# Performance work log

Measured on AMD Instinct MI355X. Metric: run time of the kernel, lower is better.

Reference implementation:

```python
import jax, jax.numpy as jnp
import numpy as np
from jax import lax

B, C, H, W = 8, 128, 128, 128
KW = 9                      # conv window width (w == h == 9)
PW = (KW - 1) // 2


def _make_kernel(key):
    # torch kaiming_normal_(fan_out) on weight (C,1,KW,C): fan_out = C * KW * C
    std = float(np.sqrt(2.0 / (C * KW * C)))
    # stored directly in WIO layout: [KW, C_in, C_out]
    return (jax.random.normal(key, (KW, C, C), dtype=jnp.float32) * std)


def setup_inputs() -> dict:
    key = jax.random.key(0)
    kx, k1, k2, k3, k4 = jax.random.split(key, 5)
    x = jax.random.normal(kx, (B, C, H, W), dtype=jnp.float32)
    return {
        "x": x,
        "k_td": _make_kernel(k1),
        "k_dt": _make_kernel(k2),
        "k_lr": _make_kernel(k3),
        "k_rl": _make_kernel(k4),
    }


def _row_conv(y, K):
    # y: [B, W, C] -> 1D conv along W, full channel mixing, no bias
    return lax.conv_general_dilated(
        y, K, window_strides=(1,), padding=[(PW, PW)],
        dimension_numbers=("NWC", "WIO", "NWC"))


def _dir_scan(x, K, reverse):
    # x: [B, H, W, C]; sequential recurrence along axis 1:
    #   row[i] = row[i] + relu(conv(row[i-1]))   (row[i-1] already updated)
    if reverse:
        x = x[:, ::-1]
    def step(prev, cur):
        new = cur + jax.nn.relu(_row_conv(prev, K))
        return new, new
    first = x[:, 0]
    _, rest = lax.scan(step, first, jnp.moveaxis(x[:, 1:], 1, 0))
    out = jnp.concatenate([first[:, None], jnp.moveaxis(rest, 0, 1)], axis=1)
    if reverse:
        out = out[:, ::-1]
    return out


def reference(x, k_td, k_dt, k_lr, k_rl):
    y = jnp.transpose(x, (0, 2, 3, 1))        # [B, H, W, C]
    y = _dir_scan(y, k_td, reverse=False)      # top -> down
    y = _dir_scan(y, k_dt, reverse=True)       # down -> top
    yt = jnp.swapaxes(y, 1, 2)                 # [B, W, H, C]
    yt = _dir_scan(yt, k_lr, reverse=False)    # left -> right
    yt = _dir_scan(yt, k_rl, reverse=True)     # right -> left
    y = jnp.swapaxes(yt, 1, 2)
    return jnp.transpose(y, (0, 3, 1, 2))      # back to [B, C, H, W]
```

## Files before the change

### kernel.cpp

```cpp
#include <hip/hip_runtime.h>

#define B_   8
#define C_   128
#define HW_  128
#define KW_  9
#define BLKS 8
#define POSB 16
#define ROWS 24
#define STRD 136
#define BUFE (ROWS * STRD)
#define THREADS 512

typedef __bf16 bf16x8 __attribute__((ext_vector_type(8)));
typedef float  floatx4 __attribute__((ext_vector_type(4)));
typedef unsigned long long u64;

__device__ __forceinline__ unsigned short bf16rn(float f) {
  union { float f; unsigned u; } x; x.f = f;
  return (unsigned short)((x.u + 0x7fffu + ((x.u >> 16) & 1u)) >> 16);
}

__global__ __launch_bounds__(256) void nchw_to_nhwc(const float* __restrict__ x,
                                                    float* __restrict__ y) {
  __shared__ float tile[32][33];
  const int blk = blockIdx.x;
  const int b = blk >> 7, h = blk & 127;
  const int tx = threadIdx.x & 31, ty = threadIdx.x >> 5;
  for (int t = 0; t < 16; ++t) {
    const int c0 = (t >> 2) * 32, w0 = (t & 3) * 32;
#pragma unroll
    for (int i = 0; i < 4; ++i) {
      const int c = c0 + ty + i * 8;
      tile[ty + i * 8][tx] = x[(((long)b * C_ + c) * HW_ + h) * HW_ + w0 + tx];
    }
    __syncthreads();
#pragma unroll
    for (int i = 0; i < 4; ++i) {
      const int w = w0 + ty + i * 8;
      y[(((long)b * HW_ + h) * HW_ + w) * C_ + c0 + tx] = tile[tx][ty + i * 8];
    }
    __syncthreads();
  }
}

__global__ __launch_bounds__(256) void nhwc_to_nchw(const float* __restrict__ y,
                                                    float* __restrict__ out) {
  __shared__ float tile[32][33];
  const int blk = blockIdx.x;
  const int b = blk >> 7, h = blk & 127;
  const int tx = threadIdx.x & 31, ty = threadIdx.x >> 5;
  for (int t = 0; t < 16; ++t) {
    const int w0 = (t >> 2) * 32, c0 = (t & 3) * 32;
#pragma unroll
    for (int i = 0; i < 4; ++i) {
      const int w = w0 + ty + i * 8;
      tile[ty + i * 8][tx] = y[(((long)b * HW_ + h) * HW_ + w) * C_ + c0 + tx];
    }
    __syncthreads();
#pragma unroll
    for (int i = 0; i < 4; ++i) {
      const int c = c0 + ty + i * 8;
      out[(((long)b * C_ + c) * HW_ + h) * HW_ + w0 + tx] = tile[tx][ty + i * 8];
    }
    __syncthreads();
  }
}

__global__ __launch_bounds__(THREADS, 2) void scnn_scan_dir(
    const float* __restrict__ Kg, float* __restrict__ y,
    int* flags, u64* mb,
    const int posStride, const int sStride, const int s0, const int ds,
    const int dirIdx) {
  __shared__ unsigned short prow[2][BUFE];
  __shared__ float scratch[4 * 2 * 64 * 4];
  const int tid = threadIdx.x;
  const int bid = blockIdx.x;
  const int batch = bid & 7;
  const int blk = bid >> 3;
  const int p0 = blk * POSB;
  const int lane = tid & 63;
  const int wave = tid >> 6;
  const int kh = wave >> 2;
  const int co2 = wave & 3;
  const int l15 = lane & 15;
  const int quad = lane >> 4;
  const int ybase = batch * (HW_ * HW_ * C_);
  int* flagB = flags + (dirIdx * 8 + batch) * BLKS;

  for (int i = tid; i < 2 * BUFE / 4; i += THREADS)
    ((u64*)prow)[i] = 0ull;

  bf16x8 wfrag[2][KW_][2];
#pragma unroll
  for (int ct = 0; ct < 2; ++ct) {
    const int co0 = co2 * 16 + ct * 64;
#pragma unroll
    for (int kw = 0; kw < KW_; ++kw)
#pragma unroll
      for (int c2 = 0; c2 < 2; ++c2) {
        const int c4 = kh * 2 + c2;
        union { bf16x8 v; unsigned short u[8]; } t;
#pragma unroll
        for (int j = 0; j < 8; ++j)
          t.u[j] = bf16rn(Kg[(kw * 128 + c4 * 32 + quad * 8 + j) * 128 + co0 + l15]);
        wfrag[ct][kw][c2] = t.v;
      }
  }
  __syncthreads();

  for (int i = tid; i < ROWS * 32; i += THREADS) {
    const int row = i >> 5, cg = i & 31;
    const int pos = p0 - 4 + row;
    if (pos >= 0 && pos < HW_) {
      const floatx4 v =
          *(const floatx4*)&y[ybase + s0 * sStride + pos * posStride + cg * 4];
      union { u64 u; unsigned short s[4]; } t;
      t.s[0] = bf16rn(v[0]); t.s[1] = bf16rn(v[1]);
      t.s[2] = bf16rn(v[2]); t.s[3] = bf16rn(v[3]);
      *(u64*)&prow[0][row * STRD + cg * 4] = t.u;
    }
  }
  __syncthreads();

  int pb = 0;
#pragma unroll 1
  for (int s = 1; s < HW_; ++s) {
    const int srow = s0 + s * ds;
    const int rowb = ybase + srow * sStride;

    __syncthreads();
    if (tid == 0)
      __hip_atomic_store(&flagB[blk], s - 1, __ATOMIC_RELAXED,
                         __HIP_MEMORY_SCOPE_AGENT);
    if (s >= 2) {
      if (tid == 0 && blk > 0)
        while (__hip_atomic_load(&flagB[blk - 1], __ATOMIC_RELAXED,
                                 __HIP_MEMORY_SCOPE_AGENT) < s - 1)
          __builtin_amdgcn_s_sleep(1);
      if (tid == 1 && blk < BLKS - 1)
        while (__hip_atomic_load(&flagB[blk + 1], __ATOMIC_RELAXED,
                                 __HIP_MEMORY_SCOPE_AGENT) < s - 1)
          __builtin_amdgcn_s_sleep(1);
      __syncthreads();
      __atomic_signal_fence(__ATOMIC_SEQ_CST);
      const int par = (s - 1) & 1;
      if (tid < 256) {
        const int side = tid >> 7, p = (tid >> 5) & 3, cg = tid & 31;
        const bool doit = side ? (blk < BLKS - 1) : (blk > 0);
        if (doit) {
          const int srcB = side ? (blk + 1) : (blk - 1);
          const int srcSide = side ? 0 : 1;
          const int mbi =
              ((((batch * BLKS + srcB) * 2 + srcSide) * 2 + par) * 4 + p) * 32 + cg;
          const u64 v =
              __hip_atomic_load(&mb[mbi], __ATOMIC_RELAXED, __HIP_MEMORY_SCOPE_AGENT);
          const int row = side ? (20 + p) : p;
          *(u64*)&prow[pb][row * STRD + cg * 4] = v;
        }
      }
    }
    __syncthreads();

    floatx4 cur[2];
    if (kh == 0) {
#pragma unroll
      for (int ct = 0; ct < 2; ++ct)
        cur[ct] = *(const floatx4*)&y[rowb + (p0 + l15) * posStride +
                                      co2 * 16 + ct * 64 + quad * 4];
    }

    floatx4 acc[2];
    acc[0] = floatx4{0.f, 0.f, 0.f, 0.f};
    acc[1] = floatx4{0.f, 0.f, 0.f, 0.f};

    const unsigned short* pbase = &prow[pb][l15 * STRD + quad * 8];
#pragma unroll
    for (int kw = 0; kw < KW_; ++kw)
#pragma unroll
      for (int c2 = 0; c2 < 2; ++c2) {
        const int c4 = kh * 2 + c2;
        const bf16x8 b0 = *(const bf16x8*)(pbase + kw * STRD + c4 * 32);
        acc[0] = __builtin_amdgcn_mfma_f32_16x16x32_bf16(wfrag[0][kw][c2], b0,
                                                         acc[0], 0, 0, 0);
        acc[1] = __builtin_amdgcn_mfma_f32_16x16x32_bf16(wfrag[1][kw][c2], b0,
                                                         acc[1], 0, 0, 0);
      }

    if (kh == 1) {
#pragma unroll
      for (int ct = 0; ct < 2; ++ct)
        *(floatx4*)&scratch[((co2 * 2 + ct) * 64 + lane) * 4] = acc[ct];
    }
    __syncthreads();

    if (kh == 0) {
#pragma unroll
      for (int ct = 0; ct < 2; ++ct) {
        const floatx4 pz =
            *(const floatx4*)&scratch[((co2 * 2 + ct) * 64 + lane) * 4];
        acc[ct] += pz;
      }

      unsigned short* nxt = prow[pb ^ 1];
      const int par_w = s & 1;
#pragma unroll
      for (int ct = 0; ct < 2; ++ct) {
        const int co0 = co2 * 16 + ct * 64;
        const int pl = l15;
        const int co = co0 + quad * 4;
        const floatx4 a = acc[ct];
        const floatx4 c = cur[ct];
        floatx4 o;
        o[0] = c[0] + (a[0] > 0.f ? a[0] : 0.f);
        o[1] = c[1] + (a[1] > 0.f ? a[1] : 0.f);
        o[2] = c[2] + (a[2] > 0.f ? a[2] : 0.f);
        o[3] = c[3] + (a[3] > 0.f ? a[3] : 0.f);
        *(floatx4*)&y[rowb + (p0 + pl) * posStride + co] = o;
        union { u64 u; unsigned short s[4]; } t;
        t.s[0] = bf16rn(o[0]); t.s[1] = bf16rn(o[1]);
        t.s[2] = bf16rn(o[2]); t.s[3] = bf16rn(o[3]);
        *(u64*)&nxt[(pl + 4) * STRD + co] = t.u;
        if (l15 < 4 && blk > 0) {
          const int mbi =
              ((((batch * BLKS + blk) * 2 + 0) * 2 + par_w) * 4 + l15) * 32 +
              (co2 * 4 + ct * 16 + quad);
          __hip_atomic_store(&mb[mbi], t.u, __ATOMIC_RELAXED,
                             __HIP_MEMORY_SCOPE_AGENT);
        }
        if (l15 >= 12 && blk < BLKS - 1) {
          const int mbi =
              ((((batch * BLKS + blk) * 2 + 1) * 2 + par_w) * 4 + (l15 - 12)) * 32 +
              (co2 * 4 + ct * 16 + quad);
          __hip_atomic_store(&mb[mbi], t.u, __ATOMIC_RELAXED,
                             __HIP_MEMORY_SCOPE_AGENT);
        }
      }
    }
    pb ^= 1;
  }
}

extern "C" void kernel_launch(void* const* d_in, const int* in_sizes, int n_in,
                              void* d_out, int out_size, void* d_ws, size_t ws_size,
                              hipStream_t stream) {
  const float* x = (const float*)d_in[0];
  const float* K[4] = {(const float*)d_in[1], (const float*)d_in[2],
                       (const float*)d_in[3], (const float*)d_in[4]};
  float* out = (float*)d_out;

  char* ws = (char*)d_ws;
  float* y = (float*)ws;
  int* flags = (int*)(ws + 67108864);
  u64* mb = (u64*)(ws + 67108864 + 1024);

  hipMemsetAsync(flags, 0, 1024, stream);
  nchw_to_nhwc<<<B_ * HW_, 256, 0, stream>>>(x, y);

  const int PS[4] = {C_, C_, HW_ * C_, HW_ * C_};
  const int SS[4] = {HW_ * C_, HW_ * C_, C_, C_};
  const int S0[4] = {0, HW_ - 1, 0, HW_ - 1};
  const int DS[4] = {1, -1, 1, -1};
  for (int d = 0; d < 4; ++d)
    scnn_scan_dir<<<B_ * BLKS, THREADS, 0, stream>>>(K[d], y, flags, mb, PS[d],
                                                     SS[d], S0[d], DS[d], d);

  nhwc_to_nchw<<<B_ * HW_, 256, 0, stream>>>(y, out);
}
```

Before: 1.986 ms.

## Overlap halo exchange with interior MFMA by splitting halo contribution

Moves the neighbor halo rows into separate shared buffers and computes the interior convolution before waiting on neighbor flags. The halo rows are then fetched by dedicated waves and their contribution is added with extra MFMAs that read zeros outside the halo. This aims to hide the inter-block spin-wait and mailbox load latency behind the main MFMA work, and it removes one block-wide barrier per step. The cost is extra MFMA instructions (up to 16 more per wave per side) and added shared-memory use.

```diff
diff --git a/kernel.cpp b/kernel.cpp
--- a/kernel.cpp
+++ b/kernel.cpp
@@ -72,6 +72,9 @@
     const int posStride, const int sStride, const int s0, const int ds,
     const int dirIdx) {
   __shared__ unsigned short prow[2][BUFE];
+  __shared__ unsigned short halL[4 * 128];
+  __shared__ unsigned short halR[4 * 128];
+  __shared__ unsigned short z16[8];
   __shared__ float scratch[4 * 2 * 64 * 4];
   const int tid = threadIdx.x;
   const int bid = blockIdx.x;
@@ -89,6 +92,10 @@
 
   for (int i = tid; i < 2 * BUFE / 4; i += THREADS)
     ((u64*)prow)[i] = 0ull;
+  for (int i = tid; i < (4 * 128 * 2 + 8) / 4; i += THREADS)
+    ((u64*)halL)[i] = 0ull;
+  for (int i = tid; i < 4 * 128 / 4; i += THREADS) ((u64*)halR)[i] = 0ull;
+  if (tid < 2) ((u64*)z16)[tid] = 0ull;
 
   bf16x8 wfrag[2][KW_][2];
 #pragma unroll
@@ -117,7 +124,12 @@
       union { u64 u; unsigned short s[4]; } t;
       t.s[0] = bf16rn(v[0]); t.s[1] = bf16rn(v[1]);
       t.s[2] = bf16rn(v[2]); t.s[3] = bf16rn(v[3]);
-      *(u64*)&prow[0][row * STRD + cg * 4] = t.u;
+      if (row < 4)
+        *(u64*)&halL[row * 128 + cg * 4] = t.u;
+      else if (row >= 20)
+        *(u64*)&halR[(row - 20) * 128 + cg * 4] = t.u;
+      else
+        *(u64*)&prow[0][row * STRD + cg * 4] = t.u;
     }
   }
   __syncthreads();
@@ -132,34 +144,6 @@
     if (tid == 0)
       __hip_atomic_store(&flagB[blk], s - 1, __ATOMIC_RELAXED,
                          __HIP_MEMORY_SCOPE_AGENT);
-    if (s >= 2) {
-      if (tid == 0 && blk > 0)
-        while (__hip_atomic_load(&flagB[blk - 1], __ATOMIC_RELAXED,
-                                 __HIP_MEMORY_SCOPE_AGENT) < s - 1)
-          __builtin_amdgcn_s_sleep(1);
-      if (tid == 1 && blk < BLKS - 1)
-        while (__hip_atomic_load(&flagB[blk + 1], __ATOMIC_RELAXED,
-                                 __HIP_MEMORY_SCOPE_AGENT) < s - 1)
-          __builtin_amdgcn_s_sleep(1);
-      __syncthreads();
-      __atomic_signal_fence(__ATOMIC_SEQ_CST);
-      const int par = (s - 1) & 1;
-      if (tid < 256) {
-        const int side = tid >> 7, p = (tid >> 5) & 3, cg = tid & 31;
-        const bool doit = side ? (blk < BLKS - 1) : (blk > 0);
-        if (doit) {
-          const int srcB = side ? (blk + 1) : (blk - 1);
-          const int srcSide = side ? 0 : 1;
-          const int mbi =
-              ((((batch * BLKS + srcB) * 2 + srcSide) * 2 + par) * 4 + p) * 32 + cg;
-          const u64 v =
-              __hip_atomic_load(&mb[mbi], __ATOMIC_RELAXED, __HIP_MEMORY_SCOPE_AGENT);
-          const int row = side ? (20 + p) : p;
-          *(u64*)&prow[pb][row * STRD + cg * 4] = v;
-        }
-      }
-    }
-    __syncthreads();
 
     floatx4 cur[2];
     if (kh == 0) {
@@ -172,7 +156,6 @@
     floatx4 acc[2];
     acc[0] = floatx4{0.f, 0.f, 0.f, 0.f};
     acc[1] = floatx4{0.f, 0.f, 0.f, 0.f};
-
     const unsigned short* pbase = &prow[pb][l15 * STRD + quad * 8];
 #pragma unroll
     for (int kw = 0; kw < KW_; ++kw)
@@ -185,6 +168,76 @@
         acc[1] = __builtin_amdgcn_mfma_f32_16x16x32_bf16(wfrag[1][kw][c2], b0,
                                                          acc[1], 0, 0, 0);
       }
+
+    if (s >= 2) {
+      const int par = (s - 1) & 1;
+      if (wave == 7 && blk > 0) {
+        if (lane == 0)
+          while (__hip_atomic_load(&flagB[blk - 1], __ATOMIC_RELAXED,
+                                   __HIP_MEMORY_SCOPE_AGENT) < s - 1)
+            __builtin_amdgcn_s_sleep(1);
+        __atomic_signal_fence(__ATOMIC_SEQ_CST);
+        const int base = ((((batch * BLKS + (blk - 1)) * 2 + 1) * 2 + par) * 4) * 32;
+        const u64 v0 = __hip_atomic_load(&mb[base + lane], __ATOMIC_RELAXED,
+                                         __HIP_MEMORY_SCOPE_AGENT);
+        const u64 v1 = __hip_atomic_load(&mb[base + 64 + lane], __ATOMIC_RELAXED,
+                                         __HIP_MEMORY_SCOPE_AGENT);
+        *(u64*)&halL[(lane >> 5) * 128 + (lane & 31) * 4] = v0;
+        *(u64*)&halL[(2 + (lane >> 5)) * 128 + (lane & 31) * 4] = v1;
+      }
+      if (wave == 6 && blk < BLKS - 1) {
+        if (lane == 0)
+          while (__hip_atomic_load(&flagB[blk + 1], __ATOMIC_RELAXED,
+                                   __HIP_MEMORY_SCOPE_AGENT) < s - 1)
+            __builtin_amdgcn_s_sleep(1);
+        __atomic_signal_fence(__ATOMIC_SEQ_CST);
+        const int base = ((((batch * BLKS + (blk + 1)) * 2 + 0) * 2 + par) * 4) * 32;
+        const u64 v0 = __hip_atomic_load(&mb[base + lane], __ATOMIC_RELAXED,
+                                         __HIP_MEMORY_SCOPE_AGENT);
+        const u64 v1 = __hip_atomic_load(&mb[base + 64 + lane], __ATOMIC_RELAXED,
+                                         __HIP_MEMORY_SCOPE_AGENT);
+        *(u64*)&halR[(lane >> 5) * 128 + (lane & 31) * 4] = v0;
+        *(u64*)&halR[(2 + (lane >> 5)) * 128 + (lane & 31) * 4] = v1;
+      }
+    }
+    __syncthreads();
+
+    if (blk > 0) {
+#pragma unroll
+      for (int kw = 0; kw < 4; ++kw) {
+        const int hr = l15 + kw;
+        const bool v = hr <= 3;
+#pragma unroll
+        for (int c2 = 0; c2 < 2; ++c2) {
+          const int c4 = kh * 2 + c2;
+          const unsigned short* sp =
+              v ? &halL[hr * 128 + c4 * 32 + quad * 8] : z16;
+          const bf16x8 b = *(const bf16x8*)sp;
+          acc[0] = __builtin_amdgcn_mfma_f32_16x16x32_bf16(wfrag[0][kw][c2], b,
+                                                           acc[0], 0, 0, 0);
+          acc[1] = __builtin_amdgcn_mfma_f32_16x16x32_bf16(wfrag[1][kw][c2], b,
+                                                           acc[1], 0, 0, 0);
+        }
+      }
+    }
+    if (blk < BLKS - 1) {
+#pragma unroll
+      for (int kw = 5; kw < 9; ++kw) {
+        const int hr = l15 + kw - 20;
+        const bool v = hr >= 0;
+#pragma unroll
+        for (int c2 = 0; c2 < 2; ++c2) {
+          const int c4 = kh * 2 + c2;
+          const unsigned short* sp =
+              v ? &halR[hr * 128 + c4 * 32 + quad * 8] : z16;
+          const bf16x8 b = *(const bf16x8*)sp;
+          acc[0] = __builtin_amdgcn_mfma_f32_16x16x32_bf16(wfrag[0][kw][c2], b,
+                                                           acc[0], 0, 0, 0);
+          acc[1] = __builtin_amdgcn_mfma_f32_16x16x32_bf16(wfrag[1][kw][c2], b,
+                                                           acc[1], 0, 0, 0);
+        }
+      }
+    }
 
     if (kh == 1) {
 #pragma unroll
```

Result: faster. 1.940 ms (-2.3%).
